# Optimization experiments

Hardware: AMD Instinct MI355X
Metric: run time of the kernel (lower is better)

The kernel has to match this reference:

```python
import jax, jax.numpy as jnp
import numpy as np

N_BINS = 65
OUTPUT_SIZE = 65


def setup_inputs() -> dict:
    key = jax.random.key(0)
    N, C, L = 512, 4, 8192
    x = jax.random.normal(key, (N, C, L), dtype=jnp.float32)
    # zero-pad head/tail so the valid-region (first..last nonzero) logic is exercised
    x = x.at[:, :, :128].set(0.0).at[:, :, L - 256:].set(0.0)
    return {"x": x}


def _mtf(x):
    N, C, L = x.shape
    nb = N_BINS

    # --- valid region: first..last nonzero per (n, c) ---
    nz = x != 0
    any_nz = nz.any(axis=-1)                                  # (N, C)
    first = jnp.argmax(nz, axis=-1)                           # (N, C)
    last = (L - 1) - jnp.argmax(nz[:, :, ::-1], axis=-1)      # (N, C)
    t = jnp.arange(L)
    mask = (t >= first[..., None]) & (t <= last[..., None]) & any_nz[..., None]

    # --- per-(n,c) quantiles over valid data (linear interpolation, like torch.quantile) ---
    big = jnp.finfo(x.dtype).max
    svals = jnp.sort(jnp.where(mask, x, big), axis=-1)        # valid values first
    m = mask.sum(axis=-1)                                      # (N, C) valid counts
    qlev = jnp.linspace(0.0, 1.0, nb + 1, dtype=x.dtype)       # (nb+1,)
    pos = qlev[None, None, :] * jnp.maximum(m - 1, 0)[..., None].astype(x.dtype)
    lo = jnp.floor(pos).astype(jnp.int32)
    hi = jnp.ceil(pos).astype(jnp.int32)
    frac = pos - lo.astype(x.dtype)
    vlo = jnp.take_along_axis(svals, lo, axis=-1)
    vhi = jnp.take_along_axis(svals, hi, axis=-1)
    q = vlo + frac * (vhi - vlo)                               # (N, C, nb+1)
    q = jnp.where((m > 0)[..., None], q, jnp.zeros_like(q))    # empty channel -> zeros

    # --- digitize: count of edges <= v  ==  searchsorted(edges, v, side='right') ---
    edges = q[:, :, :-1]                                       # (N, C, nb), sorted
    bins = jax.vmap(jax.vmap(
        lambda e, v: jnp.searchsorted(e, v, side='right')))(edges, x)
    bins = jnp.clip(bins, 0, nb - 1)                           # (N, C, L)

    # --- pairwise transition histogram via flat scatter-add ---
    cur = bins[:, :, :-1]
    nxt = bins[:, :, 1:]
    n_idx = jnp.arange(N)[:, None, None]
    c_idx = jnp.arange(C)[None, :, None]
    flat = ((n_idx * C + c_idx) * nb + cur) * nb + nxt         # (N, C, L-1)
    hist = jnp.zeros(N * C * nb * nb, dtype=x.dtype).at[flat.ravel()].add(1.0)
    mtf = hist.reshape(N, C, nb, nb) / (L - 1)

    # --- resize (identity when n_bins == output_size) ---
    size = min(nb, OUTPUT_SIZE)
    out = jnp.zeros((N, C, OUTPUT_SIZE, OUTPUT_SIZE), dtype=x.dtype)
    out = out.at[:, :, :size, :size].set(mtf[:, :, :size, :size])
    return out


def reference(x) -> jnp.ndarray:
    return _mtf(x)
```

## Files before the change

### kernel.cpp

```cpp
#include <hip/hip_runtime.h>
#include <cfloat>

constexpr int NB   = 65;
constexpr int LROW = 8192;
constexpr int NT   = 512;
constexpr int EPT  = 16;
constexpr int NBUK = 1024;

__device__ __forceinline__ int bucket_of(float v) {
    float t = (v + 6.0f) * (float(NBUK) / 12.0f);
    t = fminf(fmaxf(t, 0.0f), float(NBUK - 1));
    return (int)t;
}

__global__ __launch_bounds__(NT, 8) void mtf_kernel(const float* __restrict__ x,
                                                    float* __restrict__ out) {
    __shared__ __align__(16) float vals[LROW];
    __shared__ __align__(16) unsigned int arr[NBUK + 1];
    __shared__ unsigned int tops[64];
    __shared__ float edges[NB];
    __shared__ unsigned short ebuk[NB];
    __shared__ unsigned int wsum[8];
    __shared__ int wfirst[8];
    __shared__ int s_first, s_last;

    const int row  = blockIdx.x;
    const int tid  = threadIdx.x;
    const int lane = tid & 63;
    const int wid  = tid >> 6;
    const float* __restrict__ xr = x + (size_t)row * LROW;

    if (tid == 0) { s_first = LROW; s_last = -1; }
    #pragma unroll
    for (int q = 0; q < NBUK / NT; ++q) arr[tid + q * NT] = 0u;

    float v[EPT];
    int   bk[EPT];
    const int base = tid * EPT;
    #pragma unroll
    for (int q = 0; q < 4; ++q) {
        float4 t = *reinterpret_cast<const float4*>(xr + base + q * 4);
        v[q*4+0] = t.x; v[q*4+1] = t.y; v[q*4+2] = t.z; v[q*4+3] = t.w;
    }
    #pragma unroll
    for (int u = 0; u < EPT; ++u) bk[u] = bucket_of(v[u]);

    int lfirst = LROW, llast = -1;
    #pragma unroll
    for (int u = 0; u < EPT; ++u)
        if (v[u] != 0.0f) { lfirst = min(lfirst, base + u); llast = max(llast, base + u); }
    #pragma unroll
    for (int d = 32; d > 0; d >>= 1) {
        lfirst = min(lfirst, __shfl_xor(lfirst, d));
        llast  = max(llast,  __shfl_xor(llast,  d));
    }
    __syncthreads();
    if (lane == 0 && llast >= 0) { atomicMin(&s_first, lfirst); atomicMax(&s_last, llast); }
    __syncthreads();
    const int first = s_first, last = s_last;
    const int m = (last >= 0) ? (last - first + 1) : 0;

    if (m > 0) {
        #pragma unroll
        for (int u = 0; u < EPT; ++u) {
            int idx = base + u;
            if (idx >= first && idx <= last) atomicAdd(&arr[bk[u]], 1u);
        }
    }
    __syncthreads();

    {
        uint2 c = *reinterpret_cast<uint2*>(&arr[tid * 2]);
        unsigned own = c.x + c.y;
        unsigned inc = own;
        #pragma unroll
        for (int d = 1; d < 64; d <<= 1) {
            unsigned n = __shfl_up(inc, d);
            if (lane >= d) inc += n;
        }
        if (lane == 63) wsum[wid] = inc;
        __syncthreads();
        if (wid == 0) {
            unsigned t0 = (lane < 8) ? wsum[lane] : 0u;
            unsigned sc = t0;
            #pragma unroll
            for (int d = 1; d < 8; d <<= 1) {
                unsigned n = __shfl_up(sc, d);
                if (lane >= d) sc += n;
            }
            if (lane < 8) wsum[lane] = sc - t0;
        }
        __syncthreads();
        unsigned b0 = wsum[wid] + (inc - own);
        arr[tid*2+0] = b0;
        arr[tid*2+1] = b0 + c.x;
    }
    __syncthreads();

    if (m > 0) {
        #pragma unroll
        for (int u = 0; u < EPT; ++u) {
            int idx = base + u;
            if (idx >= first && idx <= last) {
                unsigned slot = atomicAdd(&arr[bk[u]], 1u);
                vals[slot] = v[u];
            }
        }
    }
    __syncthreads();
    if (tid < 64) tops[tid] = arr[tid * 16 + 15];
    __syncthreads();

    for (int k = wid; k < NB; k += 8) {
        if (m == 0) {
            if (lane == 0) { edges[k] = 0.0f; ebuk[k] = (unsigned short)bucket_of(0.0f); }
            continue;
        }
        const float delta = __fdiv_rn(1.0f, 65.0f);
        float qv   = __fmul_rn((float)k, delta);
        float pos  = __fmul_rn(qv, (float)(m - 1));
        float flo  = floorf(pos);
        float frac = __fsub_rn(pos, flo);
        int lo = (int)flo;
        int hi = (int)ceilf(pos);

        int bL, bH;
        {
            unsigned long long b1 = __ballot((int)tops[lane] > lo);
            int seg = __ffsll(b1) - 1;
            unsigned long long b2 = __ballot(lane < 16 && (int)arr[seg*16 + lane] > lo);
            bL = seg * 16 + __ffsll(b2) - 1;
        }
        if (hi == lo) bH = bL;
        else {
            unsigned long long b1 = __ballot((int)tops[lane] > hi);
            int seg = __ffsll(b1) - 1;
            unsigned long long b2 = __ballot(lane < 16 && (int)arr[seg*16 + lane] > hi);
            bH = seg * 16 + __ffsll(b2) - 1;
        }

        int stL = bL ? (int)arr[bL - 1] : 0;
        int enL = (int)arr[bL];
        int rlo = lo - stL, rhi = hi - stL;
        bool sameB = (bH == bL);
        float vlo = 0.0f, vhi = 0.0f;
        bool fL = false, fH = !sameB;
        for (int b0 = stL; b0 < enL; b0 += 64) {
            int i = b0 + lane;
            bool act = i < enL;
            float vi = act ? vals[i] : 0.0f;
            int cl = 0, ce = 0;
            for (int j = stL; j < enL; ++j) {
                float vj = vals[j];
                cl += (vj < vi);
                ce += (vj == vi);
            }
            if (!fL) {
                unsigned long long mk = __ballot(act && cl <= rlo && rlo < cl + ce);
                if (mk) { vlo = __shfl(vi, __ffsll(mk) - 1); fL = true; }
            }
            if (!fH) {
                unsigned long long mk = __ballot(act && cl <= rhi && rhi < cl + ce);
                if (mk) { vhi = __shfl(vi, __ffsll(mk) - 1); fH = true; }
            }
            if (fL && fH) break;
        }
        if (!sameB) {
            int stH = (int)arr[bH - 1], enH = (int)arr[bH];
            float mn = FLT_MAX;
            for (int i = stH + lane; i < enH; i += 64) mn = fminf(mn, vals[i]);
            #pragma unroll
            for (int d = 32; d > 0; d >>= 1) mn = fminf(mn, __shfl_xor(mn, d));
            vhi = mn;
        }
        float e = __fadd_rn(vlo, __fmul_rn(frac, __fsub_rn(vhi, vlo)));
        if (lane == 0) { edges[k] = e; ebuk[k] = (unsigned short)bucket_of(e); }
    }
    __syncthreads();

    unsigned int* thist = reinterpret_cast<unsigned int*>(vals);
    for (int i = tid; i < NB * NB; i += NT) thist[i] = 0u;
    for (int b = tid; b <= NBUK; b += NT) {
        int lo2 = 0, hi2 = NB;
        #pragma unroll
        for (int it = 0; it < 7; ++it) {
            if (lo2 < hi2) {
                int mid = (lo2 + hi2) >> 1;
                if ((int)ebuk[mid] < b) lo2 = mid + 1; else hi2 = mid;
            }
        }
        arr[b] = (unsigned)lo2;
    }
    __syncthreads();

    int bl[EPT];
    #pragma unroll
    for (int u = 0; u < EPT; ++u) {
        int b   = bk[u];
        int cnt = (int)arr[b];
        int en  = (int)arr[b + 1];
        for (int j = cnt; j < en; ++j) cnt += (edges[j] <= v[u]);
        bl[u] = min(cnt, NB - 1);
    }
    if (lane == 0) wfirst[wid] = bl[0];
    __syncthreads();

    int nxt0 = __shfl_down(bl[0], 1);
    if (lane == 63 && wid < 7) nxt0 = wfirst[wid + 1];
    #pragma unroll
    for (int u = 0; u + 1 < EPT; ++u)
        atomicAdd(&thist[bl[u] * NB + bl[u + 1]], 1u);
    if (tid + 1 < NT)
        atomicAdd(&thist[bl[EPT - 1] * NB + nxt0], 1u);
    __syncthreads();

    float* __restrict__ orow = out + (size_t)row * (NB * NB);
    for (int i = tid; i < NB * NB; i += NT)
        orow[i] = __fdiv_rn((float)thist[i], (float)(LROW - 1));
}

extern "C" void kernel_launch(void* const* d_in, const int* in_sizes, int n_in,
                              void* d_out, int out_size, void* d_ws, size_t ws_size,
                              hipStream_t stream) {
    const float* x = (const float*)d_in[0];
    float* out = (float*)d_out;
    const int rows = in_sizes[0] / LROW;
    mtf_kernel<<<rows, NT, 0, stream>>>(x, out);
}
```

Before: 186.5 us.

## Scatter only values in buckets containing quantile positions; recompute buckets instead of storing

Finds the buckets holding each quantile's lo/hi ranks right after the prefix scan, marks them in a bitmap, and scatters only values from marked buckets into shared memory. This avoids scattering all ~8K values with LDS atomics when only about 65 buckets are needed. It also drops the per-thread bucket array and recomputes bucket_of on demand, which lowers register pressure at the cost of extra ALU work. Bucket ranges are cached per quantile in a small shared struct.

```diff
diff --git a/kernel.cpp b/kernel.cpp
--- a/kernel.cpp
+++ b/kernel.cpp
@@ -12,6 +12,8 @@
     t = fminf(fmaxf(t, 0.0f), float(NBUK - 1));
     return (int)t;
 }
+
+struct ERange { unsigned short stL, enL, stH, enH; };
 
 __global__ __launch_bounds__(NT, 8) void mtf_kernel(const float* __restrict__ x,
                                                     float* __restrict__ out) {
@@ -20,6 +22,8 @@
     __shared__ unsigned int tops[64];
     __shared__ float edges[NB];
     __shared__ unsigned short ebuk[NB];
+    __shared__ ERange erng[NB];
+    __shared__ unsigned int bmap[NBUK / 32];
     __shared__ unsigned int wsum[8];
     __shared__ int wfirst[8];
     __shared__ int s_first, s_last;
@@ -33,17 +37,15 @@
     if (tid == 0) { s_first = LROW; s_last = -1; }
     #pragma unroll
     for (int q = 0; q < NBUK / NT; ++q) arr[tid + q * NT] = 0u;
+    if (tid < NBUK / 32) bmap[tid] = 0u;
 
     float v[EPT];
-    int   bk[EPT];
     const int base = tid * EPT;
     #pragma unroll
     for (int q = 0; q < 4; ++q) {
         float4 t = *reinterpret_cast<const float4*>(xr + base + q * 4);
         v[q*4+0] = t.x; v[q*4+1] = t.y; v[q*4+2] = t.z; v[q*4+3] = t.w;
     }
-    #pragma unroll
-    for (int u = 0; u < EPT; ++u) bk[u] = bucket_of(v[u]);
 
     int lfirst = LROW, llast = -1;
     #pragma unroll
@@ -64,7 +66,7 @@
         #pragma unroll
         for (int u = 0; u < EPT; ++u) {
             int idx = base + u;
-            if (idx >= first && idx <= last) atomicAdd(&arr[bk[u]], 1u);
+            if (idx >= first && idx <= last) atomicAdd(&arr[bucket_of(v[u])], 1u);
         }
     }
     __syncthreads();
@@ -94,6 +96,41 @@
         unsigned b0 = wsum[wid] + (inc - own);
         arr[tid*2+0] = b0;
         arr[tid*2+1] = b0 + c.x;
+        if (tid == NT - 1) arr[NBUK] = b0 + own;
+    }
+    __syncthreads();
+    if (tid < 64) tops[tid] = arr[tid * 16 + 16];
+    __syncthreads();
+
+    const float delta = __fdiv_rn(1.0f, 65.0f);
+    for (int k = wid; k < NB; k += 8) {
+        if (m == 0) continue;
+        float qv  = __fmul_rn((float)k, delta);
+        float pos = __fmul_rn(qv, (float)(m - 1));
+        int lo = (int)floorf(pos);
+        int hi = (int)ceilf(pos);
+        int bL, bH;
+        {
+            unsigned long long b1 = __ballot((int)tops[lane] > lo);
+            int seg = __ffsll(b1) - 1;
+            unsigned long long b2 = __ballot(lane < 16 && (int)arr[seg*16 + lane + 1] > lo);
+            bL = seg * 16 + __ffsll(b2) - 1;
+        }
+        if (hi == lo) bH = bL;
+        else {
+            unsigned long long b1 = __ballot((int)tops[lane] > hi);
+            int seg = __ffsll(b1) - 1;
+            unsigned long long b2 = __ballot(lane < 16 && (int)arr[seg*16 + lane + 1] > hi);
+            bH = seg * 16 + __ffsll(b2) - 1;
+        }
+        if (lane == 0) {
+            ERange e;
+            e.stL = (unsigned short)arr[bL]; e.enL = (unsigned short)arr[bL + 1];
+            e.stH = (unsigned short)arr[bH]; e.enH = (unsigned short)arr[bH + 1];
+            erng[k] = e;
+            atomicOr(&bmap[bL >> 5], 1u << (bL & 31));
+            atomicOr(&bmap[bH >> 5], 1u << (bH & 31));
+        }
     }
     __syncthreads();
 
@@ -102,13 +139,14 @@
         for (int u = 0; u < EPT; ++u) {
             int idx = base + u;
             if (idx >= first && idx <= last) {
-                unsigned slot = atomicAdd(&arr[bk[u]], 1u);
-                vals[slot] = v[u];
-            }
-        }
-    }
-    __syncthreads();
-    if (tid < 64) tops[tid] = arr[tid * 16 + 15];
+                int b = bucket_of(v[u]);
+                if ((bmap[b >> 5] >> (b & 31)) & 1u) {
+                    unsigned slot = atomicAdd(&arr[b], 1u);
+                    vals[slot] = v[u];
+                }
+            }
+        }
+    }
     __syncthreads();
 
     for (int k = wid; k < NB; k += 8) {
@@ -116,33 +154,16 @@
             if (lane == 0) { edges[k] = 0.0f; ebuk[k] = (unsigned short)bucket_of(0.0f); }
             continue;
         }
-        const float delta = __fdiv_rn(1.0f, 65.0f);
         float qv   = __fmul_rn((float)k, delta);
         float pos  = __fmul_rn(qv, (float)(m - 1));
         float flo  = floorf(pos);
         float frac = __fsub_rn(pos, flo);
         int lo = (int)flo;
         int hi = (int)ceilf(pos);
-
-        int bL, bH;
-        {
-            unsigned long long b1 = __ballot((int)tops[lane] > lo);
-            int seg = __ffsll(b1) - 1;
-            unsigned long long b2 = __ballot(lane < 16 && (int)arr[seg*16 + lane] > lo);
-            bL = seg * 16 + __ffsll(b2) - 1;
-        }
-        if (hi == lo) bH = bL;
-        else {
-            unsigned long long b1 = __ballot((int)tops[lane] > hi);
-            int seg = __ffsll(b1) - 1;
-            unsigned long long b2 = __ballot(lane < 16 && (int)arr[seg*16 + lane] > hi);
-            bH = seg * 16 + __ffsll(b2) - 1;
-        }
-
-        int stL = bL ? (int)arr[bL - 1] : 0;
-        int enL = (int)arr[bL];
+        ERange e = erng[k];
+        int stL = e.stL, enL = e.enL;
         int rlo = lo - stL, rhi = hi - stL;
-        bool sameB = (bH == bL);
+        bool sameB = (e.stH == e.stL);
         float vlo = 0.0f, vhi = 0.0f;
         bool fL = false, fH = !sameB;
         for (int b0 = stL; b0 < enL; b0 += 64) {
@@ -166,15 +187,14 @@
             if (fL && fH) break;
         }
         if (!sameB) {
-            int stH = (int)arr[bH - 1], enH = (int)arr[bH];
             float mn = FLT_MAX;
-            for (int i = stH + lane; i < enH; i += 64) mn = fminf(mn, vals[i]);
+            for (int i = e.stH + lane; i < e.enH; i += 64) mn = fminf(mn, vals[i]);
             #pragma unroll
             for (int d = 32; d > 0; d >>= 1) mn = fminf(mn, __shfl_xor(mn, d));
             vhi = mn;
         }
-        float e = __fadd_rn(vlo, __fmul_rn(frac, __fsub_rn(vhi, vlo)));
-        if (lane == 0) { edges[k] = e; ebuk[k] = (unsigned short)bucket_of(e); }
+        float ev = __fadd_rn(vlo, __fmul_rn(frac, __fsub_rn(vhi, vlo)));
+        if (lane == 0) { edges[k] = ev; ebuk[k] = (unsigned short)bucket_of(ev); }
     }
     __syncthreads();
 
@@ -196,7 +216,7 @@
     int bl[EPT];
     #pragma unroll
     for (int u = 0; u < EPT; ++u) {
-        int b   = bk[u];
+        int b   = bucket_of(v[u]);
         int cnt = (int)arr[b];
         int en  = (int)arr[b + 1];
         for (int j = cnt; j < en; ++j) cnt += (edges[j] <= v[u]);
```

After: 174.1 us. -6.7%, faster.
